# Kernel optimization log

Measured on AMD Instinct MI355X. Metric: run time of the kernel, lower is better.

The kernel has to match this reference:

```python
import jax, jax.numpy as jnp
import numpy as np

N, M, D = 1024, 32, 512


def setup_inputs() -> dict:
    key = jax.random.key(0)
    kx, = jax.random.split(key, 1)
    x = jax.random.normal(kx, (N, M, D), dtype=jnp.float32)
    w = jnp.asarray(10.0, dtype=jnp.float32)
    b = jnp.asarray(-5.0, dtype=jnp.float32)
    return {"x": x, "w": w, "b": b}


def reference(x, w, b):
    # x: (N, M, D) d-vectors. GE2E softmax loss (Wan et al. 2018, Eq. 6).
    n, m, d = x.shape
    centroids = x.mean(axis=1)                      # (N, D)
    # leave-one-out centroid for each (speaker, utt): (sum - x_ji) / (M-1)
    excl = (x.sum(axis=1, keepdims=True) - x) / (m - 1)  # (N, M, D)

    x_norm = jnp.linalg.norm(x, axis=-1)            # (N, M)
    c_norm = jnp.linalg.norm(centroids, axis=-1)    # (N,)
    e_norm = jnp.linalg.norm(excl, axis=-1)         # (N, M)

    # cosine sim vs all full centroids: (N, M, N)
    cos_all = jnp.einsum('nmd,kd->nmk', x, centroids) / (
        x_norm[..., None] * c_norm[None, None, :])
    # cosine sim vs own leave-one-out centroid: (N, M)
    cos_own = (x * excl).sum(axis=-1) / (x_norm * e_norm)

    # replace the k == speaker column with the leave-one-out similarity
    own_col = jnp.eye(n, dtype=bool)[:, None, :]    # (N, 1, N)
    cs = jnp.where(own_col, cos_own[..., None], cos_all)
    cs = jnp.maximum(cs, 1e-6)                      # torch.clamp(., 1e-06)
    cs = w * cs + b

    logp = jax.nn.log_softmax(cs, axis=-1)          # (N, M, N)
    # L[j, i] = -logp[j, i, j]
    L = -jnp.diagonal(logp, axis1=0, axis2=2).T     # (N, M)
    return L.mean()
```

## Files before the change

### kernel.cpp

```cpp
#include <hip/hip_runtime.h>
#include <hip/hip_bf16.h>
#include <hip/hip_fp8.h>
#include <math.h>

#define GN 1024
#define GM 32
#define GD 512
#define NROW (GN*GM)

#define WS_XF8   0ull
#define WS_SF8   16777216ull
#define WS_INVSN 17301504ull
#define WS_INVXN 17305600ull
#define WS_CSOWN 17436672ull
#define WS_PS    17567744ull

typedef __attribute__((ext_vector_type(2))) long i64x2;
typedef __attribute__((ext_vector_type(4))) float f32x4;

__device__ inline unsigned char f32_to_e4m3(float f) {
    __hip_fp8_e4m3 q(f);
    return (unsigned char)q.__x;
}

__device__ inline int img_off(int k) {
    const int rem = k & 63;
    return (k & ~63) + ((rem >> 3) & 3) * 16 + (rem >> 5) * 8 + (rem & 7);
}

__global__ __launch_bounds__(512) void prep_kernel(
    const float* __restrict__ x, const float* __restrict__ wp,
    const float* __restrict__ bp, char* __restrict__ wsb)
{
    unsigned char* xf8 = (unsigned char*)(wsb + WS_XF8);
    unsigned char* Sf8 = (unsigned char*)(wsb + WS_SF8);
    float* invSn = (float*)(wsb + WS_INVSN);
    float* invxn = (float*)(wsb + WS_INVXN);
    float* csown = (float*)(wsb + WS_CSOWN);

    const int n = blockIdx.x;
    const int d = threadIdx.x;
    const int lane = d & 63;
    const int wid  = d >> 6;

    __shared__ float sx[GM][GD];
    __shared__ float sS[GD];
    __shared__ float red[8];
    __shared__ float sSn2;

    const float* xn_ = x + (size_t)n * GM * GD;
    const int off = img_off(d);

    float Sd = 0.f;
    #pragma unroll
    for (int m = 0; m < GM; ++m) {
        float xv = xn_[m * GD + d];
        sx[m][d] = xv;
        Sd += xv;
        xf8[(size_t)(n * GM + m) * GD + off] = f32_to_e4m3(xv);
    }
    sS[d] = Sd;
    Sf8[(size_t)n * GD + off] = f32_to_e4m3(Sd);

    float p = Sd * Sd;
    #pragma unroll
    for (int o = 32; o > 0; o >>= 1) p += __shfl_down(p, o);
    if (lane == 0) red[wid] = p;
    __syncthreads();
    if (d == 0) {
        float s = 0.f;
        #pragma unroll
        for (int i = 0; i < 8; ++i) s += red[i];
        sSn2 = s;
        invSn[n] = rsqrtf(s);
    }
    __syncthreads();

    const float w0 = wp[0], b0 = bp[0];
    const float Sn2 = sSn2;
    #pragma unroll
    for (int mm = 0; mm < 4; ++mm) {
        const int m = wid + mm * 8;
        float xn2 = 0.f, dn = 0.f;
        #pragma unroll
        for (int j = 0; j < 8; ++j) {
            float xv = sx[m][lane + 64 * j];
            float sv = sS[lane + 64 * j];
            xn2 += xv * xv;
            dn  += xv * sv;
        }
        #pragma unroll
        for (int o = 32; o > 0; o >>= 1) {
            xn2 += __shfl_down(xn2, o);
            dn  += __shfl_down(dn, o);
        }
        if (lane == 0) {
            float ixn = rsqrtf(xn2);
            float en2 = Sn2 - 2.f * dn + xn2;
            float cosown = (dn - xn2) * ixn * rsqrtf(en2);
            csown[n * GM + m] = w0 * fmaxf(cosown, 1e-6f) + b0;
            invxn[n * GM + m] = ixn;
        }
    }
}

__global__ __launch_bounds__(256, 4) void gemm_kernel(
    const float* __restrict__ wp, const float* __restrict__ bp,
    char* __restrict__ wsb)
{
    const unsigned char* xf8 = (const unsigned char*)(wsb + WS_XF8);
    const unsigned char* Sf8 = (const unsigned char*)(wsb + WS_SF8);
    const float* invSn = (const float*)(wsb + WS_INVSN);
    const float* invxn = (const float*)(wsb + WS_INVXN);
    const float* csown = (const float*)(wsb + WS_CSOWN);
    float* ps = (float*)(wsb + WS_PS);

    __shared__ __align__(16) unsigned char Ab[2][256][16];
    __shared__ __align__(16) unsigned char Bb[2][512][16];

    const int bid  = blockIdx.x;
    const int u    = bid >> 3;
    const int rowp = (bid & 7) * 64 + (u >> 3);
    const int colp = u & 7;
    const int rbase = rowp * 64;
    const int cbase = colp * 128;

    const int t    = threadIdx.x;
    const int w    = t >> 6;
    const int lane = t & 63;
    const int wr   = w >> 1, wc = w & 1;

    const int kb  = lane >> 4;
    const int r16 = lane & 15;

    f32x4 acc[2][4] = {};

    const unsigned char* agbase = xf8 + (size_t)(rbase + (t & 63)) * GD + (t >> 6) * 16;
    const unsigned char* bgbase = Sf8 + (size_t)(cbase + (t & 127)) * GD + (t >> 7) * 16;
    const int wbase = w * 64;

#define STAGE(buf, ks)                                                        \
    do {                                                                      \
        const int kof_ = (ks) * 64;                                           \
        __builtin_amdgcn_global_load_lds(                                     \
            (const __attribute__((address_space(1))) void*)(agbase + kof_),   \
            (__attribute__((address_space(3))) void*)&Ab[buf][wbase][0],      \
            16, 0, 0);                                                        \
        __builtin_amdgcn_global_load_lds(                                     \
            (const __attribute__((address_space(1))) void*)(bgbase + kof_),   \
            (__attribute__((address_space(3))) void*)&Bb[buf][wbase][0],      \
            16, 0, 0);                                                        \
        __builtin_amdgcn_global_load_lds(                                     \
            (const __attribute__((address_space(1))) void*)(bgbase + kof_ + 32), \
            (__attribute__((address_space(3))) void*)&Bb[buf][256 + wbase][0],\
            16, 0, 0);                                                        \
    } while (0)

    auto compute = [&](int buf) {
        i64x2 af[2], bfr[4];
        #pragma unroll
        for (int mi = 0; mi < 2; ++mi)
            af[mi] = *(const i64x2*)&Ab[buf][kb * 64 + wr * 32 + mi * 16 + r16][0];
        #pragma unroll
        for (int nj = 0; nj < 4; ++nj)
            bfr[nj] = *(const i64x2*)&Bb[buf][kb * 128 + wc * 64 + nj * 16 + r16][0];
        #pragma unroll
        for (int mi = 0; mi < 2; ++mi)
            #pragma unroll
            for (int nj = 0; nj < 4; ++nj) {
                acc[mi][nj] = __builtin_amdgcn_mfma_f32_16x16x32_fp8_fp8(
                    af[mi][0], bfr[nj][0], acc[mi][nj], 0, 0, 0);
                acc[mi][nj] = __builtin_amdgcn_mfma_f32_16x16x32_fp8_fp8(
                    af[mi][1], bfr[nj][1], acc[mi][nj], 0, 0, 0);
            }
    };

#define WAITVM0()  asm volatile("s_waitcnt vmcnt(0)" ::: "memory")
#define BARRIER()  asm volatile("s_barrier" ::: "memory")

#define KSTEP(ks)                                                             \
    do {                                                                      \
        WAITVM0();                                                            \
        BARRIER();                                                            \
        if ((ks) + 1 < 8) STAGE(((ks) + 1) & 1, (ks) + 1);                    \
        compute((ks) & 1);                                                    \
    } while (0)

    STAGE(0, 0);

    KSTEP(0);  KSTEP(1);  KSTEP(2);  KSTEP(3);
    KSTEP(4);  KSTEP(5);  KSTEP(6);  KSTEP(7);

#undef KSTEP
#undef WAITVM0
#undef BARRIER
#undef STAGE

    const float w0 = wp[0], b0 = bp[0];
    const float C = fmaxf(w0 * 1e-6f + b0, w0 + b0);
    const int pcol = colp * 2 + wc;
    float isn[4];
    #pragma unroll
    for (int nj = 0; nj < 4; ++nj)
        isn[nj] = invSn[cbase + wc * 64 + nj * 16 + r16];

    #pragma unroll
    for (int mi = 0; mi < 2; ++mi) {
        #pragma unroll
        for (int r = 0; r < 4; ++r) {
            const int row = rbase + wr * 32 + mi * 16 + kb * 4 + r;
            const float ixn = invxn[row];
            const float cso = csown[row];
            const int own = row >> 5;
            float se = 0.f;
            #pragma unroll
            for (int nj = 0; nj < 4; ++nj) {
                const int col = cbase + wc * 64 + nj * 16 + r16;
                float cs = w0 * fmaxf(acc[mi][nj][r] * ixn * isn[nj], 1e-6f) + b0;
                cs = (col == own) ? cso : cs;
                se += __expf(cs - C);
            }
            #pragma unroll
            for (int off = 1; off < 16; off <<= 1)
                se += __shfl_xor(se, off, 16);
            if (r16 == 0)
                ps[(size_t)row * 16 + pcol] = se;
        }
    }
}

__global__ __launch_bounds__(256) void finalize_kernel(
    const char* __restrict__ wsb, const float* __restrict__ wp,
    const float* __restrict__ bp, float* __restrict__ out)
{
    const float* csown = (const float*)(wsb + WS_CSOWN);
    const float* ps    = (const float*)(wsb + WS_PS);

    const float w0 = wp[0], b0 = bp[0];
    const float C = fmaxf(w0 * 1e-6f + b0, w0 + b0);

    const int row = blockIdx.x * 256 + threadIdx.x;
    float s = 0.f;
    #pragma unroll
    for (int i = 0; i < 16; ++i) s += ps[(size_t)row * 16 + i];
    float loss = C + logf(s) - csown[row];

    const int lane = threadIdx.x & 63;
    const int wid  = threadIdx.x >> 6;
    __shared__ float red[4];
    #pragma unroll
    for (int off = 32; off > 0; off >>= 1) loss += __shfl_down(loss, off);
    if (lane == 0) red[wid] = loss;
    __syncthreads();
    if (threadIdx.x == 0) {
        float sum = red[0] + red[1] + red[2] + red[3];
        atomicAdd(out, sum * (1.f / (GN * GM)));
    }
}

extern "C" void kernel_launch(void* const* d_in, const int* in_sizes, int n_in,
                              void* d_out, int out_size, void* d_ws, size_t ws_size,
                              hipStream_t stream)
{
    const float* x  = (const float*)d_in[0];
    const float* wp = (const float*)d_in[1];
    const float* bp = (const float*)d_in[2];
    float* out = (float*)d_out;
    char* wsb  = (char*)d_ws;

    hipMemsetAsync(d_out, 0, sizeof(float), stream);

    prep_kernel<<<GN, 512, 0, stream>>>(x, wp, bp, wsb);

    gemm_kernel<<<4096, 256, 0, stream>>>(wp, bp, wsb);

    finalize_kernel<<<128, 256, 0, stream>>>(wsb, wp, bp, out);
}
```

Measured before the change: 88.03 us.

## Switch GEMM to 32x32x64 scaled FP8 MFMA with 128-row tiles

Replaces the 16x16x32 FP8 MFMA path with the gfx950 32x32x64 f8f6f4 scaled MFMA (unit scales), so each instruction covers more work and fewer LDS fragment loads are needed. The block tile grows from 64 to 128 rows, which halves the grid and doubles the A staging buffer. The prep kernel now writes FP8 data in plain row-major order, and the LDS staging and epilogue row/column mapping follow the 32x32 accumulator layout. The cost is more registers per thread (occupancy hint removed) and fewer blocks in flight.

```diff
diff --git a/kernel.cpp b/kernel.cpp
--- a/kernel.cpp
+++ b/kernel.cpp
@@ -15,17 +15,13 @@
 #define WS_CSOWN 17436672ull
 #define WS_PS    17567744ull
 
-typedef __attribute__((ext_vector_type(2))) long i64x2;
-typedef __attribute__((ext_vector_type(4))) float f32x4;
+typedef __attribute__((ext_vector_type(4)))  int   i32x4;
+typedef __attribute__((ext_vector_type(8)))  int   i32x8;
+typedef __attribute__((ext_vector_type(16))) float f32x16;
 
 __device__ inline unsigned char f32_to_e4m3(float f) {
     __hip_fp8_e4m3 q(f);
     return (unsigned char)q.__x;
-}
-
-__device__ inline int img_off(int k) {
-    const int rem = k & 63;
-    return (k & ~63) + ((rem >> 3) & 3) * 16 + (rem >> 5) * 8 + (rem & 7);
 }
 
 __global__ __launch_bounds__(512) void prep_kernel(
@@ -49,7 +45,6 @@
     __shared__ float sSn2;
 
     const float* xn_ = x + (size_t)n * GM * GD;
-    const int off = img_off(d);
 
     float Sd = 0.f;
     #pragma unroll
@@ -57,10 +52,10 @@
         float xv = xn_[m * GD + d];
         sx[m][d] = xv;
         Sd += xv;
-        xf8[(size_t)(n * GM + m) * GD + off] = f32_to_e4m3(xv);
+        xf8[(size_t)(n * GM + m) * GD + d] = f32_to_e4m3(xv);
     }
     sS[d] = Sd;
-    Sf8[(size_t)n * GD + off] = f32_to_e4m3(Sd);
+    Sf8[(size_t)n * GD + d] = f32_to_e4m3(Sd);
 
     float p = Sd * Sd;
     #pragma unroll
@@ -104,7 +99,7 @@
     }
 }
 
-__global__ __launch_bounds__(256, 4) void gemm_kernel(
+__global__ __launch_bounds__(256) void gemm_kernel(
     const float* __restrict__ wp, const float* __restrict__ bp,
     char* __restrict__ wsb)
 {
@@ -115,14 +110,14 @@
     const float* csown = (const float*)(wsb + WS_CSOWN);
     float* ps = (float*)(wsb + WS_PS);
 
-    __shared__ __align__(16) unsigned char Ab[2][256][16];
+    __shared__ __align__(16) unsigned char Ab[2][512][16];
     __shared__ __align__(16) unsigned char Bb[2][512][16];
 
     const int bid  = blockIdx.x;
     const int u    = bid >> 3;
-    const int rowp = (bid & 7) * 64 + (u >> 3);
+    const int rowp = (bid & 7) * 32 + (u >> 3);
     const int colp = u & 7;
-    const int rbase = rowp * 64;
+    const int rbase = rowp * 128;
     const int cbase = colp * 128;
 
     const int t    = threadIdx.x;
@@ -130,49 +125,59 @@
     const int lane = t & 63;
     const int wr   = w >> 1, wc = w & 1;
 
-    const int kb  = lane >> 4;
-    const int r16 = lane & 15;
-
-    f32x4 acc[2][4] = {};
-
-    const unsigned char* agbase = xf8 + (size_t)(rbase + (t & 63)) * GD + (t >> 6) * 16;
-    const unsigned char* bgbase = Sf8 + (size_t)(cbase + (t & 127)) * GD + (t >> 7) * 16;
-    const int wbase = w * 64;
+    f32x16 acc[2][2] = {};
+
+    const int srow = w * 32 + (t & 31);
+    const int ah   = ((t >> 5) & 1) * 32;
+    const unsigned char* agbase = xf8 + (size_t)(rbase + srow) * GD + ah;
+    const unsigned char* bgbase = Sf8 + (size_t)(cbase + srow) * GD + ah;
+    const int cb0 = w * 64;
+    const int cb1 = 256 + w * 64;
 
 #define STAGE(buf, ks)                                                        \
     do {                                                                      \
         const int kof_ = (ks) * 64;                                           \
         __builtin_amdgcn_global_load_lds(                                     \
             (const __attribute__((address_space(1))) void*)(agbase + kof_),   \
-            (__attribute__((address_space(3))) void*)&Ab[buf][wbase][0],      \
+            (__attribute__((address_space(3))) void*)&Ab[buf][cb0][0],        \
+            16, 0, 0);                                                        \
+        __builtin_amdgcn_global_load_lds(                                     \
+            (const __attribute__((address_space(1))) void*)(agbase + kof_ + 16), \
+            (__attribute__((address_space(3))) void*)&Ab[buf][cb1][0],        \
             16, 0, 0);                                                        \
         __builtin_amdgcn_global_load_lds(                                     \
             (const __attribute__((address_space(1))) void*)(bgbase + kof_),   \
-            (__attribute__((address_space(3))) void*)&Bb[buf][wbase][0],      \
-            16, 0, 0);                                                        \
-        __builtin_amdgcn_global_load_lds(                                     \
-            (const __attribute__((address_space(1))) void*)(bgbase + kof_ + 32), \
-            (__attribute__((address_space(3))) void*)&Bb[buf][256 + wbase][0],\
+            (__attribute__((address_space(3))) void*)&Bb[buf][cb0][0],        \
+            16, 0, 0);                                                        \
+        __builtin_amdgcn_global_load_lds(                                     \
+            (const __attribute__((address_space(1))) void*)(bgbase + kof_ + 16), \
+            (__attribute__((address_space(3))) void*)&Bb[buf][cb1][0],        \
             16, 0, 0);                                                        \
     } while (0)
 
     auto compute = [&](int buf) {
-        i64x2 af[2], bfr[4];
-        #pragma unroll
-        for (int mi = 0; mi < 2; ++mi)
-            af[mi] = *(const i64x2*)&Ab[buf][kb * 64 + wr * 32 + mi * 16 + r16][0];
-        #pragma unroll
-        for (int nj = 0; nj < 4; ++nj)
-            bfr[nj] = *(const i64x2*)&Bb[buf][kb * 128 + wc * 64 + nj * 16 + r16][0];
+        i32x8 af[2], bf[2];
+        #pragma unroll
+        for (int mi = 0; mi < 2; ++mi) {
+            const int s = wr * 2 + mi;
+            i32x4 lo = *(const i32x4*)&Ab[buf][s * 64 + lane][0];
+            i32x4 hi = *(const i32x4*)&Ab[buf][256 + s * 64 + lane][0];
+            af[mi] = __builtin_shufflevector(lo, hi, 0, 1, 2, 3, 4, 5, 6, 7);
+        }
+        #pragma unroll
+        for (int nj = 0; nj < 2; ++nj) {
+            const int s = wc * 2 + nj;
+            i32x4 lo = *(const i32x4*)&Bb[buf][s * 64 + lane][0];
+            i32x4 hi = *(const i32x4*)&Bb[buf][256 + s * 64 + lane][0];
+            bf[nj] = __builtin_shufflevector(lo, hi, 0, 1, 2, 3, 4, 5, 6, 7);
+        }
         #pragma unroll
         for (int mi = 0; mi < 2; ++mi)
             #pragma unroll
-            for (int nj = 0; nj < 4; ++nj) {
-                acc[mi][nj] = __builtin_amdgcn_mfma_f32_16x16x32_fp8_fp8(
-                    af[mi][0], bfr[nj][0], acc[mi][nj], 0, 0, 0);
-                acc[mi][nj] = __builtin_amdgcn_mfma_f32_16x16x32_fp8_fp8(
-                    af[mi][1], bfr[nj][1], acc[mi][nj], 0, 0, 0);
-            }
+            for (int nj = 0; nj < 2; ++nj)
+                acc[mi][nj] = __builtin_amdgcn_mfma_scale_f32_32x32x64_f8f6f4(
+                    af[mi], bf[nj], acc[mi][nj], 0, 0,
+                    0, 0x7F7F7F7F, 0, 0x7F7F7F7F);
     };
 
 #define WAITVM0()  asm volatile("s_waitcnt vmcnt(0)" ::: "memory")
@@ -199,31 +204,34 @@
     const float w0 = wp[0], b0 = bp[0];
     const float C = fmaxf(w0 * 1e-6f + b0, w0 + b0);
     const int pcol = colp * 2 + wc;
-    float isn[4];
-    #pragma unroll
-    for (int nj = 0; nj < 4; ++nj)
-        isn[nj] = invSn[cbase + wc * 64 + nj * 16 + r16];
+    const int h   = lane >> 5;
+    const int c31 = lane & 31;
+    float isn[2];
+    #pragma unroll
+    for (int nj = 0; nj < 2; ++nj)
+        isn[nj] = invSn[cbase + wc * 64 + nj * 32 + c31];
 
     #pragma unroll
     for (int mi = 0; mi < 2; ++mi) {
         #pragma unroll
-        for (int r = 0; r < 4; ++r) {
-            const int row = rbase + wr * 32 + mi * 16 + kb * 4 + r;
+        for (int r = 0; r < 16; ++r) {
+            const int row = rbase + wr * 64 + mi * 32
+                          + (r & 3) + 8 * (r >> 2) + 4 * h;
             const float ixn = invxn[row];
             const float cso = csown[row];
             const int own = row >> 5;
             float se = 0.f;
             #pragma unroll
-            for (int nj = 0; nj < 4; ++nj) {
-                const int col = cbase + wc * 64 + nj * 16 + r16;
+            for (int nj = 0; nj < 2; ++nj) {
+                const int col = cbase + wc * 64 + nj * 32 + c31;
                 float cs = w0 * fmaxf(acc[mi][nj][r] * ixn * isn[nj], 1e-6f) + b0;
                 cs = (col == own) ? cso : cs;
                 se += __expf(cs - C);
             }
             #pragma unroll
-            for (int off = 1; off < 16; off <<= 1)
-                se += __shfl_xor(se, off, 16);
-            if (r16 == 0)
+            for (int off = 1; off < 32; off <<= 1)
+                se += __shfl_xor(se, off);
+            if (c31 == 0)
                 ps[(size_t)row * 16 + pcol] = se;
         }
     }
@@ -272,7 +280,7 @@
 
     prep_kernel<<<GN, 512, 0, stream>>>(x, wp, bp, wsb);
 
-    gemm_kernel<<<4096, 256, 0, stream>>>(wp, bp, wsb);
+    gemm_kernel<<<2048, 256, 0, stream>>>(wp, bp, wsb);
 
     finalize_kernel<<<128, 256, 0, stream>>>(wsb, wp, bp, out);
 }
```

Result: slower. 161.8 us (+83.7%).
